# Optimization experiments

Measured on AMD Instinct MI355X. Metric: run time of the kernel, lower is better.

The kernel has to match this reference:

```python
import jax, jax.numpy as jnp
import numpy as np

N, E, F_IN, H, C = 50000, 800000, 256, 64, 40
NEG_SLOPE = 0.2


def setup_inputs() -> dict:
    key = jax.random.key(0)
    ks = jax.random.split(key, 16)
    sc = lambda fan: 1.0 / np.sqrt(fan)
    return {
        "x": jax.random.normal(ks[0], (N, F_IN), dtype=jnp.float32),
        "edge_index": jax.random.randint(ks[1], (2, E), 0, N, dtype=jnp.int64),
        "W1l": jax.random.normal(ks[2], (F_IN, H), dtype=jnp.float32) * sc(F_IN),
        "b1l": jnp.zeros((H,), jnp.float32),
        "W1r": jax.random.normal(ks[3], (F_IN, H), dtype=jnp.float32) * sc(F_IN),
        "b1r": jnp.zeros((H,), jnp.float32),
        "att1": jax.random.normal(ks[4], (H,), dtype=jnp.float32) * sc(H),
        "bias1": jnp.zeros((H,), jnp.float32),
        "lin1_W": jax.random.normal(ks[5], (F_IN, H), dtype=jnp.float32) * sc(F_IN),
        "lin1_b": jnp.zeros((H,), jnp.float32),
        "W2l": jax.random.normal(ks[6], (H, C), dtype=jnp.float32) * sc(H),
        "b2l": jnp.zeros((C,), jnp.float32),
        "W2r": jax.random.normal(ks[7], (H, C), dtype=jnp.float32) * sc(H),
        "b2r": jnp.zeros((C,), jnp.float32),
        "att2": jax.random.normal(ks[8], (C,), dtype=jnp.float32) * sc(C),
        "bias2": jnp.zeros((C,), jnp.float32),
        "lin2_W": jax.random.normal(ks[9], (H, C), dtype=jnp.float32) * sc(H),
        "lin2_b": jnp.zeros((C,), jnp.float32),
    }


def gatv2_layer(x, src, dst, Wl, bl, Wr, br, att, bias, n):
    # PyG GATv2Conv, heads=1: xl = lin_l(x) (source), xr = lin_r(x) (target)
    xl = x @ Wl + bl                               # [n, out]
    xr = x @ Wr + br                               # [n, out]
    m = xl[src] + xr[dst]                          # [E, out] per-edge gather
    e = jax.nn.leaky_relu(m, NEG_SLOPE) @ att      # [E] attention logits
    # segment softmax over destination nodes (self-loops guarantee nonempty segments)
    emax = jax.ops.segment_max(e, dst, num_segments=n)
    ee = jnp.exp(e - emax[dst])
    denom = jax.ops.segment_sum(ee, dst, num_segments=n)
    alpha = ee / denom[dst]                        # [E]
    out = jax.ops.segment_sum(alpha[:, None] * xl[src], dst, num_segments=n)
    return out + bias


def reference(x, edge_index, W1l, b1l, W1r, b1r, att1, bias1, lin1_W, lin1_b,
              W2l, b2l, W2r, b2r, att2, bias2, lin2_W, lin2_b):
    n = x.shape[0]
    loops = jnp.arange(n, dtype=edge_index.dtype)
    src = jnp.concatenate([edge_index[0], loops])  # add_self_loops=True (PyG default)
    dst = jnp.concatenate([edge_index[1], loops])
    h = jax.nn.relu(gatv2_layer(x, src, dst, W1l, b1l, W1r, b1r, att1, bias1, n)
                    + x @ lin1_W + lin1_b)
    o = (gatv2_layer(h, src, dst, W2l, b2l, W2r, b2r, att2, bias2, n)
         + h @ lin2_W + lin2_b)
    return jax.nn.log_softmax(o, axis=1), edge_index
```

## Files before the change

kernel.cpp:

```cpp
#include <hip/hip_runtime.h>
#include <cmath>

#define NN 50000
#define NP 50048
#define NE 800000
#define CD 40
#define NEG_SLOPE 0.2f
#define NITEMS (NE + NN)
#define CHUNK 2048
#define NCH 416
#define NBKT 391
#define BCAP 3072
#define GB1 782
#define TB1 (3 * 64 * 256)
#define TB2 (3 * 64 * 64)
#define WPB 240

typedef __attribute__((ext_vector_type(8))) short s16x8;
typedef __attribute__((ext_vector_type(4))) float f32x4;
typedef __attribute__((ext_vector_type(2))) float f32x2;

__device__ __forceinline__ f32x2 pk_fma(f32x2 a, f32x2 b, f32x2 c) {
#if __has_builtin(__builtin_elementwise_fma)
  return __builtin_elementwise_fma(a, b, c);
#else
  f32x2 r; r[0] = fmaf(a[0], b[0], c[0]); r[1] = fmaf(a[1], b[1], c[1]); return r;
#endif
}
__device__ __forceinline__ f32x2 pk_max(f32x2 a, f32x2 b) {
#if __has_builtin(__builtin_elementwise_max)
  return __builtin_elementwise_max(a, b);
#else
  f32x2 r; r[0] = fmaxf(a[0], b[0]); r[1] = fmaxf(a[1], b[1]); return r;
#endif
}

__device__ __forceinline__ short f2bf(float x) {
  unsigned u = __builtin_bit_cast(unsigned, x);
  u += 0x7fffu + ((u >> 16) & 1u);
  return (short)(u >> 16);
}
__device__ __forceinline__ unsigned pack2(float lo, float hi) {
  return (unsigned)(unsigned short)f2bf(lo) | ((unsigned)(unsigned short)f2bf(hi) << 16);
}
__device__ __forceinline__ float bf2f_lo(unsigned v) {
  return __builtin_bit_cast(float, v << 16);
}
__device__ __forceinline__ float bf2f_hi(unsigned v) {
  return __builtin_bit_cast(float, v & 0xffff0000u);
}
__device__ __forceinline__ void unp8(uint4 v, f32x2* f) {
  f[0] = (f32x2){bf2f_lo(v.x), bf2f_hi(v.x)};
  f[1] = (f32x2){bf2f_lo(v.y), bf2f_hi(v.y)};
  f[2] = (f32x2){bf2f_lo(v.z), bf2f_hi(v.z)};
  f[3] = (f32x2){bf2f_lo(v.w), bf2f_hi(v.w)};
}
__device__ __forceinline__ uint4 zero4() {
  uint4 z; z.x = 0u; z.y = 0u; z.z = 0u; z.w = 0u; return z;
}

__global__ __launch_bounds__(256) void prep_bin(const float* __restrict__ W1l,
                                                const float* __restrict__ W1r,
                                                const float* __restrict__ L1,
                                                const float* __restrict__ W2l,
                                                const float* __restrict__ W2r,
                                                const float* __restrict__ L2,
                                                short* __restrict__ Wp1,
                                                short* __restrict__ Wp2,
                                                const int* __restrict__ ei,
                                                float* __restrict__ outE,
                                                int* __restrict__ gcur,
                                                unsigned* __restrict__ rec) {
  const int tid = threadIdx.x;
  if (blockIdx.x < WPB) {
    int e = blockIdx.x * 256 + tid;
    if (e < TB1) {
      int kb = e / 6144, r = e % 6144;
      int w = r / 2048, r2 = r % 2048;
      int t = r2 / 512, r3 = r2 % 512;
      int lane = r3 / 8, j = r3 % 8;
      int n = t * 16 + (lane & 15);
      int k = kb * 32 + (lane >> 4) * 8 + j;
      const float* W = (w == 0) ? W1l : (w == 1) ? W1r : L1;
      Wp1[e] = f2bf(W[k * 64 + n]);
    } else {
      e -= TB1;
      int kb = e / 6144, r = e % 6144;
      int w = r / 2048, r2 = r % 2048;
      int t = r2 / 512, r3 = r2 % 512;
      int lane = r3 / 8, j = r3 % 8;
      int n = t * 16 + (lane & 15);
      int k = kb * 32 + (lane >> 4) * 8 + j;
      const float* W = (w == 0) ? W2l : (w == 1) ? W2r : L2;
      Wp2[e] = (n < 40) ? f2bf(W[k * 40 + n]) : (short)0;
    }
    return;
  }
  __shared__ unsigned sorted[CHUNK];
  __shared__ int hist[512];
  __shared__ int bcur[512];
  __shared__ int gbase[512];
  const int base = (blockIdx.x - WPB) * CHUNK;
  for (int t = tid; t < 512; t += 256) { hist[t] = 0; bcur[t] = 0; gbase[t] = 0; }
  __syncthreads();
  unsigned key[CHUNK / 256];
#pragma unroll
  for (int u = 0; u < CHUNK / 256; ++u) {
    const int j = base + u * 256 + tid;
    unsigned k = 0xFFFFFFFFu;
    if (j < NITEMS) {
      int s, d;
      if (j < NE) {
        s = ei[j]; d = ei[NE + j];
        outE[j] = (float)s; outE[NE + j] = (float)d;
      } else {
        s = j - NE; d = s;
      }
      k = ((unsigned)d << 16) | (unsigned)s;
      atomicAdd(&hist[k >> 23], 1);
    }
    key[u] = k;
  }
  __syncthreads();
  if (tid < 64) {
    int carry = 0;
#pragma unroll
    for (int c = 0; c < 8; ++c) {
      int v = hist[c * 64 + tid];
      int inc = v;
#pragma unroll
      for (int off = 1; off < 64; off <<= 1) {
        int tt = __shfl_up(inc, off, 64);
        if (tid >= off) inc += tt;
      }
      hist[c * 64 + tid] = carry + inc - v;
      carry += __shfl(inc, 63, 64);
    }
  }
  __syncthreads();
#pragma unroll
  for (int u = 0; u < CHUNK / 256; ++u) {
    const unsigned k = key[u];
    if (k != 0xFFFFFFFFu) {
      const int b = k >> 23;
      sorted[hist[b] + atomicAdd(&bcur[b], 1)] = k;
    }
  }
  __syncthreads();
  for (int t = tid; t < NBKT; t += 256) {
    const int c = bcur[t];
    if (c > 0) gbase[t] = atomicAdd(&gcur[t], c);
  }
  __syncthreads();
  const int cnt = min(CHUNK, NITEMS - base);
  for (int i = tid; i < cnt; i += 256) {
    const unsigned k = sorted[i];
    const int b = k >> 23;
    const int p = gbase[b] + (i - hist[b]);
    if (p < BCAP) rec[(size_t)b * BCAP + p] = k;
  }
}

__device__ __forceinline__ void gemm1_body(int bid, const float* __restrict__ X,
                                           const short* __restrict__ Wp,
                                           const float* __restrict__ B0,
                                           const float* __restrict__ B1,
                                           const float* __restrict__ B2,
                                           unsigned short* __restrict__ Y0,
                                           unsigned short* __restrict__ Y1,
                                           unsigned short* __restrict__ Y2) {
  const int lane = threadIdx.x & 63;
  const int wave = threadIdx.x >> 6;
  const int r0 = bid * 64 + wave * 16;
  const int m = lane & 15;
  const int q = lane >> 4;
  f32x4 acc[3][4] = {};
  const float* a0 = X + (size_t)min(r0 + m, NN - 1) * 256 + q * 8;
  const short* bp = Wp + lane * 8;
  float4 v0 = *reinterpret_cast<const float4*>(a0);
  float4 v1 = *reinterpret_cast<const float4*>(a0 + 4);
#pragma unroll
  for (int kb = 0; kb < 8; ++kb) {
    s16x8 bf[12];
#pragma unroll
    for (int i = 0; i < 12; ++i)
      bf[i] = *reinterpret_cast<const s16x8*>(bp + (size_t)(kb * 12 + i) * 512);
    s16x8 af;
    af[0] = f2bf(v0.x); af[1] = f2bf(v0.y); af[2] = f2bf(v0.z); af[3] = f2bf(v0.w);
    af[4] = f2bf(v1.x); af[5] = f2bf(v1.y); af[6] = f2bf(v1.z); af[7] = f2bf(v1.w);
    if (kb < 7) {
      v0 = *reinterpret_cast<const float4*>(a0 + (kb + 1) * 32);
      v1 = *reinterpret_cast<const float4*>(a0 + (kb + 1) * 32 + 4);
    }
#pragma unroll
    for (int i = 0; i < 12; ++i)
      acc[i >> 2][i & 3] = __builtin_amdgcn_mfma_f32_16x16x32_bf16(
          af, bf[i], acc[i >> 2][i & 3], 0, 0, 0);
  }
#pragma unroll
  for (int w = 0; w < 3; ++w) {
    const float* B = (w == 0) ? B0 : (w == 1) ? B1 : B2;
    unsigned short* Y = (w == 0) ? Y0 : (w == 1) ? Y1 : Y2;
#pragma unroll
    for (int t = 0; t < 4; ++t) {
      const int c = t * 16 + m;
      const float bv = B[c];
#pragma unroll
      for (int rg = 0; rg < 4; ++rg) {
        const int row = r0 + q * 4 + rg;
        if (row < NN)
          Y[(size_t)row * 64 + c] = (unsigned short)f2bf(acc[w][t][rg] + bv);
      }
    }
  }
}

__global__ __launch_bounds__(256, 2) void build_gemm1(
    const float* __restrict__ X, const short* __restrict__ Wp1,
    const float* __restrict__ B0, const float* __restrict__ B1,
    const float* __restrict__ B2, unsigned short* __restrict__ Y0,
    unsigned short* __restrict__ Y1, unsigned short* __restrict__ Y2,
    const int* __restrict__ gcur, const unsigned* __restrict__ rec,
    int* __restrict__ offsets, unsigned short* __restrict__ csr16) {
  if (blockIdx.x < GB1) {
    gemm1_body(blockIdx.x, X, Wp1, B0, B1, B2, Y0, Y1, Y2);
    return;
  }
  const int b = blockIdx.x - GB1;
  const int tid = threadIdx.x;
  __shared__ unsigned recs[BCAP];
  __shared__ int red[256];
  __shared__ int cnt[128];
  __shared__ int sc[128];
  __shared__ int cur[128];
  int acc = 0;
  for (int t = tid; t < NBKT; t += 256)
    if (t < b) acc += gcur[t];
  red[tid] = acc;
  __syncthreads();
#pragma unroll
  for (int off = 128; off >= 1; off >>= 1) {
    if (tid < off) red[tid] += red[tid + off];
    __syncthreads();
  }
  const int base = red[0];
  const int Tb = min(gcur[b], BCAP);
  if (tid < 128) cnt[tid] = 0;
  __syncthreads();
  for (int i = tid; i < Tb; i += 256) {
    const unsigned k = rec[(size_t)b * BCAP + i];
    recs[i] = k;
    atomicAdd(&cnt[(k >> 16) & 127], 1);
  }
  __syncthreads();
  if (tid < 128) sc[tid] = cnt[tid];
  __syncthreads();
#pragma unroll
  for (int off = 1; off < 128; off <<= 1) {
    int v = (tid < 128 && tid >= off) ? sc[tid - off] : 0;
    __syncthreads();
    if (tid < 128) sc[tid] += v;
    __syncthreads();
  }
  if (tid < 128) {
    const int n = b * 128 + tid;
    if (n < NN) offsets[n + 1] = base + sc[tid];
    cur[tid] = sc[tid] - cnt[tid];
  }
  if (b == 0 && tid == 0) offsets[0] = 0;
  __syncthreads();
  for (int i = tid; i < Tb; i += 256) {
    const unsigned k = recs[i];
    const int p = atomicAdd(&cur[(k >> 16) & 127], 1);
    csr16[base + p] = (unsigned short)(k & 0xFFFFu);
  }
}

__global__ __launch_bounds__(256, 2) void gemm2(const short* __restrict__ Xb,
                                                const short* __restrict__ Wp,
                                                const float* __restrict__ B0,
                                                const float* __restrict__ B1,
                                                const float* __restrict__ B2,
                                                unsigned short* __restrict__ Y0,
                                                unsigned short* __restrict__ Y1,
                                                unsigned short* __restrict__ Y2) {
  const int lane = threadIdx.x & 63;
  const int wave = threadIdx.x >> 6;
  const int r0 = blockIdx.x * 64 + wave * 16;
  const int m = lane & 15;
  const int q = lane >> 4;
  f32x4 acc[3][3] = {};
  const short* a0 = Xb + (size_t)(r0 + m) * 64 + q * 8;
  const short* bp = Wp + lane * 8;
#pragma unroll
  for (int kb = 0; kb < 2; ++kb) {
    s16x8 bf[9];
#pragma unroll
    for (int w = 0; w < 3; ++w)
#pragma unroll
      for (int t = 0; t < 3; ++t)
        bf[w * 3 + t] =
            *reinterpret_cast<const s16x8*>(bp + (size_t)(kb * 12 + w * 4 + t) * 512);
    const s16x8 af = *reinterpret_cast<const s16x8*>(a0 + kb * 32);
#pragma unroll
    for (int w = 0; w < 3; ++w)
#pragma unroll
      for (int t = 0; t < 3; ++t)
        acc[w][t] = __builtin_amdgcn_mfma_f32_16x16x32_bf16(af, bf[w * 3 + t],
                                                            acc[w][t], 0, 0, 0);
  }
#pragma unroll
  for (int w = 0; w < 3; ++w) {
    const float* B = (w == 0) ? B0 : (w == 1) ? B1 : B2;
    unsigned short* Y = (w == 0) ? Y0 : (w == 1) ? Y1 : Y2;
#pragma unroll
    for (int t = 0; t < 3; ++t) {
      const int c = t * 16 + m;
      if (c < 40) {
        const float bv = B[c];
#pragma unroll
        for (int rg = 0; rg < 4; ++rg) {
          const int row = r0 + q * 4 + rg;
          if (row < NN)
            Y[(size_t)row * 64 + c] = (unsigned short)f2bf(acc[w][t][rg] + bv);
        }
      }
    }
  }
}

template <int OC, bool FINAL>
__global__ __launch_bounds__(256) void gat_agg(const unsigned short* __restrict__ XL,
                                               const unsigned short* __restrict__ XR,
                                               const unsigned short* __restrict__ XLIN,
                                               const float* __restrict__ att,
                                               const float* __restrict__ bias,
                                               const int* __restrict__ offsets,
                                               const unsigned short* __restrict__ csr,
                                               float* __restrict__ out,
                                               unsigned short* __restrict__ outb) {
  const int lane = threadIdx.x & 63;
  const int g = lane >> 3;
  const int l = lane & 7;
  const int wv = threadIdx.x >> 6;
  const int d = (blockIdx.x * 4 + wv) * 8 + g;
  const int dd = min(d, NN - 1);
  constexpr bool FULLW = (OC >= 64);
  const bool dimok = FULLW || (8 * l < OC);

  const int beg = offsets[dd];
  int end = offsets[dd + 1];
  if (d >= NN) end = beg;
  const int deg = end - beg;
  int mdeg = deg;
  mdeg = max(mdeg, __shfl_xor(mdeg, 8, 64));
  mdeg = max(mdeg, __shfl_xor(mdeg, 16, 64));
  mdeg = max(mdeg, __shfl_xor(mdeg, 32, 64));

  f32x2 a2[4] = {};
  if (dimok) {
    const float4 t0 = *reinterpret_cast<const float4*>(&att[8 * l]);
    const float4 t1 = *reinterpret_cast<const float4*>(&att[8 * l + 4]);
    a2[0] = (f32x2){t0.x, t0.y}; a2[1] = (f32x2){t0.z, t0.w};
    a2[2] = (f32x2){t1.x, t1.y}; a2[3] = (f32x2){t1.z, t1.w};
  }
  f32x2 xr2[4];
  unp8(dimok ? *reinterpret_cast<const uint4*>(XR + (size_t)dd * 64 + 8 * l) : zero4(),
       xr2);

  const unsigned short* XLl = XL + 8 * l;
  float D = 0.f;
  f32x2 A2[4] = {};
  const f32x2 ns = (f32x2){NEG_SLOPE, NEG_SLOPE};
  const int CL = NITEMS - 1;
  int sa = (int)csr[min(beg, CL)];
  uint4 rn = dimok ? *reinterpret_cast<const uint4*>(XLl + (size_t)sa * 64) : zero4();
  sa = (int)csr[min(beg + 1, CL)];
  for (int it = 0; it < mdeg; ++it) {
    const uint4 raw = rn;
    rn = dimok ? *reinterpret_cast<const uint4*>(XLl + (size_t)sa * 64) : zero4();
    sa = (int)csr[min(beg + it + 2, CL)];
    f32x2 xl2[4];
    unp8(raw, xl2);
    f32x2 pacc = (f32x2){0.f, 0.f};
#pragma unroll
    for (int j = 0; j < 4; ++j) {
      const f32x2 t = xl2[j] + xr2[j];
      const f32x2 lr = pk_max(t, t * ns);
      pacc = pk_fma(lr, a2[j], pacc);
    }
    float p = pacc[0] + pacc[1];
    p += __shfl_xor(p, 1, 64);
    p += __shfl_xor(p, 2, 64);
    p += __shfl_xor(p, 4, 64);
    const float w = (it < deg) ? __expf(p) : 0.f;
    D += w;
    const f32x2 w2 = (f32x2){w, w};
#pragma unroll
    for (int j = 0; j < 4; ++j) A2[j] = pk_fma(w2, xl2[j], A2[j]);
  }
  if (d >= NN) return;
  f32x2 xlin2[4];
  unp8(dimok ? *reinterpret_cast<const uint4*>(XLIN + (size_t)dd * 64 + 8 * l)
             : zero4(),
       xlin2);
  float b[8] = {};
  if (dimok) {
    const float4 t0 = *reinterpret_cast<const float4*>(&bias[8 * l]);
    const float4 t1 = *reinterpret_cast<const float4*>(&bias[8 * l + 4]);
    b[0] = t0.x; b[1] = t0.y; b[2] = t0.z; b[3] = t0.w;
    b[4] = t1.x; b[5] = t1.y; b[6] = t1.z; b[7] = t1.w;
  }
  const float inv = 1.0f / D;
  float val[8];
#pragma unroll
  for (int j = 0; j < 8; ++j)
    val[j] = fmaf(A2[j >> 1][j & 1], inv, b[j]) + xlin2[j >> 1][j & 1];
  if (!FINAL) {
    uint4 o;
    o.x = pack2(fmaxf(val[0], 0.f), fmaxf(val[1], 0.f));
    o.y = pack2(fmaxf(val[2], 0.f), fmaxf(val[3], 0.f));
    o.z = pack2(fmaxf(val[4], 0.f), fmaxf(val[5], 0.f));
    o.w = pack2(fmaxf(val[6], 0.f), fmaxf(val[7], 0.f));
    *reinterpret_cast<uint4*>(&outb[(size_t)d * 64 + 8 * l]) = o;
  } else {
    float mx = -3e38f;
    if (dimok) {
#pragma unroll
      for (int j = 0; j < 8; ++j) mx = fmaxf(mx, val[j]);
    }
    mx = fmaxf(mx, __shfl_xor(mx, 1, 64));
    mx = fmaxf(mx, __shfl_xor(mx, 2, 64));
    mx = fmaxf(mx, __shfl_xor(mx, 4, 64));
    float es = 0.f;
    if (dimok) {
#pragma unroll
      for (int j = 0; j < 8; ++j) es += __expf(val[j] - mx);
    }
    es += __shfl_xor(es, 1, 64);
    es += __shfl_xor(es, 2, 64);
    es += __shfl_xor(es, 4, 64);
    const float lse = mx + __logf(es);
    if (dimok) {
      float4 o0, o1;
      o0.x = val[0] - lse; o0.y = val[1] - lse; o0.z = val[2] - lse; o0.w = val[3] - lse;
      o1.x = val[4] - lse; o1.y = val[5] - lse; o1.z = val[6] - lse; o1.w = val[7] - lse;
      float* dst = &out[(size_t)d * OC + 8 * l];
      *reinterpret_cast<float4*>(dst) = o0;
      *reinterpret_cast<float4*>(dst + 4) = o1;
    }
  }
}

extern "C" void kernel_launch(void* const* d_in, const int* in_sizes, int n_in,
                              void* d_out, int out_size, void* d_ws, size_t ws_size,
                              hipStream_t stream) {
  const float* x     = (const float*)d_in[0];
  const int*   ei    = (const int*)d_in[1];
  const float* W1l   = (const float*)d_in[2];
  const float* b1l   = (const float*)d_in[3];
  const float* W1r   = (const float*)d_in[4];
  const float* b1r   = (const float*)d_in[5];
  const float* att1  = (const float*)d_in[6];
  const float* bias1 = (const float*)d_in[7];
  const float* lin1W = (const float*)d_in[8];
  const float* lin1b = (const float*)d_in[9];
  const float* W2l   = (const float*)d_in[10];
  const float* b2l   = (const float*)d_in[11];
  const float* W2r   = (const float*)d_in[12];
  const float* b2r   = (const float*)d_in[13];
  const float* att2  = (const float*)d_in[14];
  const float* bias2 = (const float*)d_in[15];
  const float* lin2W = (const float*)d_in[16];
  const float* lin2b = (const float*)d_in[17];
  float* out = (float*)d_out;

  char* ws = (char*)d_ws;
  size_t off = 0;
  auto alloc = [&](size_t bytes) -> void* {
    void* p = ws + off;
    off += (bytes + 255) & ~(size_t)255;
    return p;
  };
  short* Wp1 = (short*)alloc((size_t)TB1 * 2);
  short* Wp2 = (short*)alloc((size_t)TB2 * 2);
  unsigned short* XL1   = (unsigned short*)alloc((size_t)NN * 64 * 2);
  unsigned short* XR1   = (unsigned short*)alloc((size_t)NN * 64 * 2);
  unsigned short* XLIN1 = (unsigned short*)alloc((size_t)NN * 64 * 2);
  unsigned short* Hb    = (unsigned short*)alloc((size_t)NP * 64 * 2);
  unsigned short* XL2   = (unsigned short*)alloc((size_t)NN * 64 * 2);
  unsigned short* XR2   = (unsigned short*)alloc((size_t)NN * 64 * 2);
  unsigned short* XLIN2 = (unsigned short*)alloc((size_t)NN * 64 * 2);
  int* gcur    = (int*)alloc((size_t)NBKT * 4);
  int* offsets = (int*)alloc((size_t)(NN + 1) * 4);
  unsigned* rec = (unsigned*)alloc((size_t)NBKT * BCAP * 4);
  unsigned short* csr = (unsigned short*)alloc((size_t)NITEMS * 2);

  hipMemsetAsync(gcur, 0, (size_t)NBKT * 4, stream);
  prep_bin<<<WPB + NCH, 256, 0, stream>>>(W1l, W1r, lin1W, W2l, W2r, lin2W,
                                          Wp1, Wp2, ei, out + (size_t)NN * CD,
                                          gcur, rec);
  build_gemm1<<<GB1 + NBKT, 256, 0, stream>>>(x, Wp1, b1l, b1r, lin1b,
                                              XL1, XR1, XLIN1, gcur, rec,
                                              offsets, csr);
  const int AGG_BLOCKS = (NN + 31) / 32;
  gat_agg<64, false><<<AGG_BLOCKS, 256, 0, stream>>>(XL1, XR1, XLIN1, att1,
                                                     bias1, offsets, csr,
                                                     nullptr, Hb);
  gemm2<<<GB1, 256, 0, stream>>>((const short*)Hb, Wp2, b2l, b2r, lin2b,
                                 XL2, XR2, XLIN2);
  gat_agg<40, true><<<AGG_BLOCKS, 256, 0, stream>>>(XL2, XR2, XLIN2, att2,
                                                    bias2, offsets, csr,
                                                    out, nullptr);
}
```

Measured before the change: 232.5 us.

## Sort nodes by degree for aggregation and pre-convert X to bf16

Builds a degree histogram during CSR construction plus a new perm_build kernel that orders destination nodes by degree (counting sort). Both aggregation kernels then read nodes through this permutation, so that the 8 nodes sharing a wave have similar degrees and less of the wave sits idle in the per-edge loop. Separately, X is converted to bf16 in extra blocks of prep_bin, so the first GEMM loads bf16 directly instead of converting fp32 in its inner loop. The cost is an extra kernel launch, an extra 25.6MB write plus read of the bf16 copy of X, and scattered node order in the aggregation, which makes XR/XLIN accesses and output writes less coalesced.

```diff
diff --git a/kernel.cpp b/kernel.cpp
--- a/kernel.cpp
+++ b/kernel.cpp
@@ -15,6 +15,8 @@
 #define TB1 (3 * 64 * 256)
 #define TB2 (3 * 64 * 64)
 #define WPB 240
+#define XCB 6250
+#define PBB 196
 
 typedef __attribute__((ext_vector_type(8))) short s16x8;
 typedef __attribute__((ext_vector_type(4))) float f32x4;
@@ -70,8 +72,20 @@
                                                 const int* __restrict__ ei,
                                                 float* __restrict__ outE,
                                                 int* __restrict__ gcur,
-                                                unsigned* __restrict__ rec) {
+                                                unsigned* __restrict__ rec,
+                                                const float* __restrict__ X,
+                                                short* __restrict__ Xb) {
   const int tid = threadIdx.x;
+  if (blockIdx.x >= WPB + NCH) {
+    const size_t e0 = ((size_t)(blockIdx.x - WPB - NCH) * 256 + tid) * 8;
+    const float4 u0 = *reinterpret_cast<const float4*>(X + e0);
+    const float4 u1 = *reinterpret_cast<const float4*>(X + e0 + 4);
+    s16x8 o;
+    o[0] = f2bf(u0.x); o[1] = f2bf(u0.y); o[2] = f2bf(u0.z); o[3] = f2bf(u0.w);
+    o[4] = f2bf(u1.x); o[5] = f2bf(u1.y); o[6] = f2bf(u1.z); o[7] = f2bf(u1.w);
+    *reinterpret_cast<s16x8*>(Xb + e0) = o;
+    return;
+  }
   if (blockIdx.x < WPB) {
     int e = blockIdx.x * 256 + tid;
     if (e < TB1) {
@@ -161,7 +175,7 @@
   }
 }
 
-__device__ __forceinline__ void gemm1_body(int bid, const float* __restrict__ X,
+__device__ __forceinline__ void gemm1_body(int bid, const short* __restrict__ Xb,
                                            const short* __restrict__ Wp,
                                            const float* __restrict__ B0,
                                            const float* __restrict__ B1,
@@ -175,23 +189,15 @@
   const int m = lane & 15;
   const int q = lane >> 4;
   f32x4 acc[3][4] = {};
-  const float* a0 = X + (size_t)min(r0 + m, NN - 1) * 256 + q * 8;
+  const short* a0 = Xb + (size_t)min(r0 + m, NN - 1) * 256 + q * 8;
   const short* bp = Wp + lane * 8;
-  float4 v0 = *reinterpret_cast<const float4*>(a0);
-  float4 v1 = *reinterpret_cast<const float4*>(a0 + 4);
 #pragma unroll
   for (int kb = 0; kb < 8; ++kb) {
+    const s16x8 af = *reinterpret_cast<const s16x8*>(a0 + kb * 32);
     s16x8 bf[12];
 #pragma unroll
     for (int i = 0; i < 12; ++i)
       bf[i] = *reinterpret_cast<const s16x8*>(bp + (size_t)(kb * 12 + i) * 512);
-    s16x8 af;
-    af[0] = f2bf(v0.x); af[1] = f2bf(v0.y); af[2] = f2bf(v0.z); af[3] = f2bf(v0.w);
-    af[4] = f2bf(v1.x); af[5] = f2bf(v1.y); af[6] = f2bf(v1.z); af[7] = f2bf(v1.w);
-    if (kb < 7) {
-      v0 = *reinterpret_cast<const float4*>(a0 + (kb + 1) * 32);
-      v1 = *reinterpret_cast<const float4*>(a0 + (kb + 1) * 32 + 4);
-    }
 #pragma unroll
     for (int i = 0; i < 12; ++i)
       acc[i >> 2][i & 3] = __builtin_amdgcn_mfma_f32_16x16x32_bf16(
@@ -216,14 +222,15 @@
 }
 
 __global__ __launch_bounds__(256, 2) void build_gemm1(
-    const float* __restrict__ X, const short* __restrict__ Wp1,
+    const short* __restrict__ Xb, const short* __restrict__ Wp1,
     const float* __restrict__ B0, const float* __restrict__ B1,
     const float* __restrict__ B2, unsigned short* __restrict__ Y0,
     unsigned short* __restrict__ Y1, unsigned short* __restrict__ Y2,
     const int* __restrict__ gcur, const unsigned* __restrict__ rec,
-    int* __restrict__ offsets, unsigned short* __restrict__ csr16) {
+    int* __restrict__ offsets, unsigned short* __restrict__ csr16,
+    int* __restrict__ dhist) {
   if (blockIdx.x < GB1) {
-    gemm1_body(blockIdx.x, X, Wp1, B0, B1, B2, Y0, Y1, Y2);
+    gemm1_body(blockIdx.x, Xb, Wp1, B0, B1, B2, Y0, Y1, Y2);
     return;
   }
   const int b = blockIdx.x - GB1;
@@ -253,7 +260,11 @@
     atomicAdd(&cnt[(k >> 16) & 127], 1);
   }
   __syncthreads();
-  if (tid < 128) sc[tid] = cnt[tid];
+  if (tid < 128) {
+    sc[tid] = cnt[tid];
+    const int n = b * 128 + tid;
+    if (n < NN) atomicAdd(&dhist[min(cnt[tid], 511)], 1);
+  }
   __syncthreads();
 #pragma unroll
   for (int off = 1; off < 128; off <<= 1) {
@@ -273,6 +284,52 @@
     const unsigned k = recs[i];
     const int p = atomicAdd(&cur[(k >> 16) & 127], 1);
     csr16[base + p] = (unsigned short)(k & 0xFFFFu);
+  }
+}
+
+__global__ __launch_bounds__(256) void perm_build(const int* __restrict__ offsets,
+                                                  const int* __restrict__ dhist,
+                                                  int* __restrict__ gcursor,
+                                                  int* __restrict__ perm) {
+  const int tid = threadIdx.x;
+  __shared__ int sbase[512];
+  __shared__ int lh[512];
+  __shared__ int lcur[512];
+  __shared__ int lbase[512];
+  for (int t = tid; t < 512; t += 256) {
+    sbase[t] = dhist[t]; lh[t] = 0; lcur[t] = 0;
+  }
+  __syncthreads();
+  if (tid < 64) {
+    int carry = 0;
+#pragma unroll
+    for (int c = 0; c < 8; ++c) {
+      int v = sbase[c * 64 + tid];
+      int inc = v;
+#pragma unroll
+      for (int off = 1; off < 64; off <<= 1) {
+        int tt = __shfl_up(inc, off, 64);
+        if (tid >= off) inc += tt;
+      }
+      sbase[c * 64 + tid] = carry + inc - v;
+      carry += __shfl(inc, 63, 64);
+    }
+  }
+  __syncthreads();
+  const int n = blockIdx.x * 256 + tid;
+  int bin = -1;
+  if (n < NN) {
+    const int deg = offsets[n + 1] - offsets[n];
+    bin = min(deg, 511);
+    atomicAdd(&lh[bin], 1);
+  }
+  __syncthreads();
+  for (int t = tid; t < 512; t += 256)
+    if (lh[t] > 0) lbase[t] = atomicAdd(&gcursor[t], lh[t]);
+  __syncthreads();
+  if (n < NN) {
+    const int p = atomicAdd(&lcur[bin], 1);
+    perm[sbase[bin] + lbase[bin] + p] = n;
   }
 }
 
@@ -337,20 +394,21 @@
                                                const float* __restrict__ bias,
                                                const int* __restrict__ offsets,
                                                const unsigned short* __restrict__ csr,
+                                               const int* __restrict__ perm,
                                                float* __restrict__ out,
                                                unsigned short* __restrict__ outb) {
   const int lane = threadIdx.x & 63;
   const int g = lane >> 3;
   const int l = lane & 7;
   const int wv = threadIdx.x >> 6;
-  const int d = (blockIdx.x * 4 + wv) * 8 + g;
-  const int dd = min(d, NN - 1);
+  const int gid = (blockIdx.x * 4 + wv) * 8 + g;
+  const int d = perm[min(gid, NN - 1)];
   constexpr bool FULLW = (OC >= 64);
   const bool dimok = FULLW || (8 * l < OC);
 
-  const int beg = offsets[dd];
-  int end = offsets[dd + 1];
-  if (d >= NN) end = beg;
+  const int beg = offsets[d];
+  int end = offsets[d + 1];
+  if (gid >= NN) end = beg;
   const int deg = end - beg;
   int mdeg = deg;
   mdeg = max(mdeg, __shfl_xor(mdeg, 8, 64));
@@ -365,7 +423,7 @@
     a2[2] = (f32x2){t1.x, t1.y}; a2[3] = (f32x2){t1.z, t1.w};
   }
   f32x2 xr2[4];
-  unp8(dimok ? *reinterpret_cast<const uint4*>(XR + (size_t)dd * 64 + 8 * l) : zero4(),
+  unp8(dimok ? *reinterpret_cast<const uint4*>(XR + (size_t)d * 64 + 8 * l) : zero4(),
        xr2);
 
   const unsigned short* XLl = XL + 8 * l;
@@ -399,9 +457,9 @@
 #pragma unroll
     for (int j = 0; j < 4; ++j) A2[j] = pk_fma(w2, xl2[j], A2[j]);
   }
-  if (d >= NN) return;
+  if (gid >= NN) return;
   f32x2 xlin2[4];
-  unp8(dimok ? *reinterpret_cast<const uint4*>(XLIN + (size_t)dd * 64 + 8 * l)
+  unp8(dimok ? *reinterpret_cast<const uint4*>(XLIN + (size_t)d * 64 + 8 * l)
              : zero4(),
        xlin2);
   float b[8] = {};
@@ -484,6 +542,7 @@
   };
   short* Wp1 = (short*)alloc((size_t)TB1 * 2);
   short* Wp2 = (short*)alloc((size_t)TB2 * 2);
+  short* Xb  = (short*)alloc((size_t)NN * 256 * 2);
   unsigned short* XL1   = (unsigned short*)alloc((size_t)NN * 64 * 2);
   unsigned short* XR1   = (unsigned short*)alloc((size_t)NN * 64 * 2);
   unsigned short* XLIN1 = (unsigned short*)alloc((size_t)NN * 64 * 2);
@@ -491,25 +550,31 @@
   unsigned short* XL2   = (unsigned short*)alloc((size_t)NN * 64 * 2);
   unsigned short* XR2   = (unsigned short*)alloc((size_t)NN * 64 * 2);
   unsigned short* XLIN2 = (unsigned short*)alloc((size_t)NN * 64 * 2);
-  int* gcur    = (int*)alloc((size_t)NBKT * 4);
+  int* meta = (int*)alloc((size_t)(NBKT + 1024) * 4);
+  int* gcur    = meta;
+  int* dhist   = meta + NBKT;
+  int* gcursor = meta + NBKT + 512;
   int* offsets = (int*)alloc((size_t)(NN + 1) * 4);
+  int* perm    = (int*)alloc((size_t)NN * 4);
   unsigned* rec = (unsigned*)alloc((size_t)NBKT * BCAP * 4);
   unsigned short* csr = (unsigned short*)alloc((size_t)NITEMS * 2);
 
-  hipMemsetAsync(gcur, 0, (size_t)NBKT * 4, stream);
-  prep_bin<<<WPB + NCH, 256, 0, stream>>>(W1l, W1r, lin1W, W2l, W2r, lin2W,
-                                          Wp1, Wp2, ei, out + (size_t)NN * CD,
-                                          gcur, rec);
-  build_gemm1<<<GB1 + NBKT, 256, 0, stream>>>(x, Wp1, b1l, b1r, lin1b,
+  hipMemsetAsync(meta, 0, (size_t)(NBKT + 1024) * 4, stream);
+  prep_bin<<<WPB + NCH + XCB, 256, 0, stream>>>(W1l, W1r, lin1W, W2l, W2r,
+                                                lin2W, Wp1, Wp2, ei,
+                                                out + (size_t)NN * CD, gcur, rec,
+                                                x, Xb);
+  build_gemm1<<<GB1 + NBKT, 256, 0, stream>>>(Xb, Wp1, b1l, b1r, lin1b,
                                               XL1, XR1, XLIN1, gcur, rec,
-                                              offsets, csr);
-  const int AGG_BLOCKS = (NN + 31) / 32;
+                                              offsets, csr, dhist);
+  perm_build<<<PBB, 256, 0, stream>>>(offsets, dhist, gcursor, perm);
+  const int AGG_BLOCKS = (NN / 8 + 3) / 4;
   gat_agg<64, false><<<AGG_BLOCKS, 256, 0, stream>>>(XL1, XR1, XLIN1, att1,
-                                                     bias1, offsets, csr,
+                                                     bias1, offsets, csr, perm,
                                                      nullptr, Hb);
   gemm2<<<GB1, 256, 0, stream>>>((const short*)Hb, Wp2, b2l, b2r, lin2b,
                                  XL2, XR2, XLIN2);
   gat_agg<40, true><<<AGG_BLOCKS, 256, 0, stream>>>(XL2, XR2, XLIN2, att2,
-                                                    bias2, offsets, csr,
+                                                    bias2, offsets, csr, perm,
                                                     out, nullptr);
 }
```

Result: slower. 380.2 us (+63.5%).
